# Performance work log

Measured on AMD Instinct MI355X. Metric: run time of the kernel, lower is better.

Reference implementation:

```python
import jax, jax.numpy as jnp
import numpy as np

EPS = 1e-5  # BatchNorm eps (eval mode: running_mean=0, running_var=1)
N, VIEWS, T, V, C_IN, H, W = 8, 4, 5, 17, 18, 16, 16
C_HID = 16


def _bn(y, g, b):
    # eval-mode BatchNorm2d on channel axis 3 of (b, g, v, c, h, w)
    s = (g / jnp.sqrt(1.0 + EPS)).reshape(1, 1, 1, -1, 1, 1)
    return y * s + b.reshape(1, 1, 1, -1, 1, 1)


def _st_gcn_layer(x, A_sp, A_tm, A_vw, Wg_k, bg_k, g1, b1, Wt_k, bt_k, g2, b2, residual):
    """One st_gcn block over 7 relation types. x: (N, Views, T, V, C, H, W)."""
    n, vw, t, v, c, h, w = x.shape
    outs = []
    for k in range(7):  # fixed small set of relations
        if k < 4:  # root/close/further/sym: graph axis is V
            xk = x.reshape(n, vw * t, v, c, h, w)
            A = A_sp[k]
        elif k < 6:  # forward/backward: graph axis is T
            xk = jnp.swapaxes(x, 2, 3).reshape(n, vw * v, t, c, h, w)
            A = A_tm[k - 4]
        else:  # n_views: graph axis is Views
            xk = jnp.swapaxes(x.reshape(n, vw, t * v, c, h, w), 1, 2)
            A = A_vw
        res = xk if residual else 0.0
        # HeatmapGraphical: 1x1 conv then adjacency aggregation over graph axis
        y = jnp.einsum('oc,bgvchw->bgvohw', Wg_k[k], xk) + bg_k[k].reshape(1, 1, 1, -1, 1, 1)
        y = jnp.einsum('uv,bgvohw->bguohw', A, y)
        # tcn: BN -> ReLU -> 1x1 conv -> BN, + residual
        y = jax.nn.relu(_bn(y, g1[k], b1[k]))
        y = jnp.einsum('oc,bgvchw->bgvohw', Wt_k[k], y) + bt_k[k].reshape(1, 1, 1, -1, 1, 1)
        y = _bn(y, g2[k], b2[k]) + res
        o = y.shape[3]
        if k < 4:
            yk = y.reshape(n, vw, t, v, o, h, w)
        elif k < 6:
            yk = jnp.swapaxes(y.reshape(n, vw, v, t, o, h, w), 2, 3)
        else:
            yk = jnp.swapaxes(y, 1, 2).reshape(n, vw, t, v, o, h, w)
        outs.append(yk)
    return jax.nn.relu(sum(outs))


def setup_inputs() -> dict:
    key = jax.random.key(0)
    ks = jax.random.split(key, 14)
    return {
        'x': jax.random.normal(ks[0], (N, VIEWS, T, V, C_IN, H, W), jnp.float32),
        'A_sp': jax.random.uniform(ks[1], (4, V, V), jnp.float32),
        'A_tm': jax.random.uniform(ks[2], (2, T, T), jnp.float32),
        'A_vw': jax.random.uniform(ks[3], (VIEWS, VIEWS), jnp.float32),
        'Wg0': jax.random.normal(ks[4], (7, C_HID, C_IN), jnp.float32) * 0.1,
        'bg0': jax.random.normal(ks[5], (7, C_HID), jnp.float32) * 0.1,
        'Wg': jax.random.normal(ks[6], (2, 7, C_HID, C_HID), jnp.float32) * 0.1,
        'bg': jax.random.normal(ks[7], (2, 7, C_HID), jnp.float32) * 0.1,
        'bn1g': jax.random.uniform(ks[8], (3, 7, C_HID), jnp.float32, 0.5, 1.5),
        'bn1b': jax.random.normal(ks[9], (3, 7, C_HID), jnp.float32) * 0.1,
        'Wt': jax.random.normal(ks[10], (3, 7, C_HID, C_HID), jnp.float32) * 0.1,
        'bt': jax.random.normal(ks[11], (3, 7, C_HID), jnp.float32) * 0.1,
        'bn2g': jax.random.uniform(ks[12], (3, 7, C_HID), jnp.float32, 0.5, 1.5),
        'bn2b': jax.random.normal(ks[13], (3, 7, C_HID), jnp.float32) * 0.1,
    }


def reference(x, A_sp, A_tm, A_vw, Wg0, bg0, Wg, bg, bn1g, bn1b, Wt, bt, bn2g, bn2b):
    # Layer 0: 18->16, residual=False (ZerosMapping)
    y = _st_gcn_layer(x, A_sp, A_tm, A_vw, Wg0, bg0, bn1g[0], bn1b[0], Wt[0], bt[0], bn2g[0], bn2b[0], residual=False)
    # Layers 1, 2: 16->16, residual=Identity
    for l in range(2):
        y = _st_gcn_layer(y, A_sp, A_tm, A_vw, Wg[l], bg[l], bn1g[l + 1], bn1b[l + 1], Wt[l + 1], bt[l + 1], bn2g[l + 1], bn2b[l + 1], residual=True)
    return y
```

## Files before the change

### kernel.cpp

```cpp
#include <hip/hip_runtime.h>
#include <hip/hip_bf16.h>

typedef __attribute__((ext_vector_type(8))) short bf16x8;
typedef __attribute__((ext_vector_type(4))) float f32x4;
typedef unsigned short ush;

constexpr int NODESV = 340, CIN = 18;
constexpr int GRP = 20;
constexpr int NSLOT = 400;
constexpr int NTILE = 25;
constexpr int RS1 = 412;
constexpr int SLX = 3208;
constexpr int SL8 = 3200;
constexpr int PC = 6120;
constexpr int PCP = 6144;
constexpr int QN = 5440;

constexpr int    WS_SB_F  = 21 * 16;
constexpr int    WS_WG    = 1536;
constexpr int    WS_WT    = WS_WG + 21 * 64 * 8 * 2;
constexpr int    WS_ASP   = WS_WT + 21 * 64 * 8 * 2;
constexpr int    WS_R16   = WS_ASP + 4096;
constexpr size_t WS_XT    = 65536;
constexpr size_t WS_NEED  = WS_XT + (size_t)8 * 256 * PCP * 2;

__device__ __forceinline__ ush f2bf(float f) {
    union { __hip_bfloat16 h; ush u; } c; c.h = __float2bfloat16(f); return c.u;
}
__device__ __forceinline__ float bf2f(ush s) {
    return __uint_as_float((unsigned)s << 16);
}
__device__ __forceinline__ unsigned pkbf2(float lo, float hi) {
    union { __hip_bfloat162 h; unsigned u; } c;
    c.h = __float22bfloat162_rn(make_float2(lo, hi));
    return c.u;
}

__global__ void stgcn_prep(
    const float* __restrict__ Asp,
    const float* __restrict__ Wg0, const float* __restrict__ bg0,
    const float* __restrict__ Wgx, const float* __restrict__ bgx,
    const float* __restrict__ g1,  const float* __restrict__ b1,
    const float* __restrict__ Wt,  const float* __restrict__ bt,
    const float* __restrict__ g2,  const float* __restrict__ b2,
    void* __restrict__ ws)
{
    const int lk = blockIdx.x;
    const int l = lk / 7, k = lk % 7;
    const int lane = threadIdx.x;
    const int o = lane & 15, quad = lane >> 4;
    float* bgvA = (float*)ws;
    float* SbA  = bgvA + WS_SB_F;
    ush* wgF = (ush*)((char*)ws + WS_WG);
    ush* wtF = (ush*)((char*)ws + WS_WT);
    const float rs = 1.0f / sqrtf(1.0f + 1e-5f);
    const float s1 = g1[lk * 16 + o] * rs;
    const float s2 = g2[lk * 16 + o] * rs;

    unsigned wg4[4], wt4[4];
    #pragma unroll
    for (int i2 = 0; i2 < 4; ++i2) {
        int c0 = quad * 8 + i2 * 2, c1 = c0 + 1;
        float a0, a1;
        if (l == 0) {
            a0 = (c0 < 18) ? Wg0[(k * 16 + o) * 18 + c0] * s1 : 0.f;
            a1 = (c1 < 18) ? Wg0[(k * 16 + o) * 18 + c1] * s1 : 0.f;
        } else {
            a0 = (c0 < 16) ? Wgx[(((l - 1) * 7 + k) * 16 + o) * 16 + c0] * s1 : 0.f;
            a1 = (c1 < 16) ? Wgx[(((l - 1) * 7 + k) * 16 + o) * 16 + c1] * s1 : 0.f;
        }
        float t0 = (c0 < 16) ? Wt[(lk * 16 + o) * 16 + c0] * s2 : 0.f;
        float t1 = (c1 < 16) ? Wt[(lk * 16 + o) * 16 + c1] * s2 : 0.f;
        wg4[i2] = pkbf2(a0, a1);
        wt4[i2] = pkbf2(t0, t1);
    }
    *(uint4*)&wgF[(lk * 64 + lane) * 8] = make_uint4(wg4[0], wg4[1], wg4[2], wg4[3]);
    *(uint4*)&wtF[(lk * 64 + lane) * 8] = make_uint4(wt4[0], wt4[1], wt4[2], wt4[3]);
    if (quad == 0)
        bgvA[lk * 16 + o] = ((l == 0) ? bg0[k * 16 + o] : bgx[((l - 1) * 7 + k) * 16 + o]) * s1;
    if (lk == 0 && lane < 48) {
        int ll = lane >> 4, ch = lane & 15;
        float s = 0.f;
        for (int kk = 0; kk < 7; ++kk) {
            int q = (ll * 7 + kk) * 16 + ch;
            s += bt[q] * (g2[q] * rs) + b2[q];
        }
        SbA[ll * 16 + ch] = s;
    }
    if (lk < 4) {
        ush* aspF = (ush*)((char*)ws + WS_ASP);
        ush* r16F = (ush*)((char*)ws + WS_R16);
        bf16x8 a0 = {};
        #pragma unroll
        for (int i = 0; i < 8; ++i) {
            int v = quad * 8 + i;
            a0[i] = (short)((v < 17) ? f2bf(Asp[(lk * 17 + o) * 17 + v]) : 0);
        }
        *(bf16x8*)&aspF[(lk * 64 + lane) * 8] = a0;
        if (lane < 32)
            r16F[lk * 32 + lane] = (lane < 17) ? f2bf(Asp[(lk * 17 + 16) * 17 + lane]) : (ush)0;
    }
}

__global__ __launch_bounds__(256) void stgcn_tin(const float* __restrict__ x,
                                                 void* __restrict__ ws)
{
    __shared__ float tf[32][256];
    const int b = blockIdx.x, tid = threadIdx.x;
    const int n = b & 7, pc0 = (b >> 3) * 32;
    for (int j = 0; j < 32; ++j) {
        int pc = pc0 + j;
        tf[j][tid] = (pc < PC) ? x[((size_t)n * PC + pc) * 256 + tid] : 0.f;
    }
    __syncthreads();
    ush* dst = (ush*)((char*)ws + WS_XT) + (size_t)(n * 256 + tid) * PCP + pc0;
    unsigned pk[16];
    #pragma unroll
    for (int j2 = 0; j2 < 16; ++j2) pk[j2] = pkbf2(tf[2 * j2][tid], tf[2 * j2 + 1][tid]);
    #pragma unroll
    for (int q4 = 0; q4 < 4; ++q4)
        *(uint4*)&dst[q4 * 8] = make_uint4(pk[q4*4], pk[q4*4+1], pk[q4*4+2], pk[q4*4+3]);
}

__global__ __launch_bounds__(256) void stgcn_tout_bf(const void* __restrict__ ws,
                                                     float* __restrict__ out)
{
    __shared__ ush tg[32][256];
    const int b = blockIdx.x, tid = threadIdx.x;
    const int n = b & 7, q0 = (b >> 3) * 32;
    const ush* src = (const ush*)((const char*)ws + WS_XT) + (size_t)(n * 256 + tid) * PCP + q0;
    #pragma unroll
    for (int j4 = 0; j4 < 4; ++j4) {
        uint4 v = *(const uint4*)&src[j4 * 8];
        unsigned u[4] = {v.x, v.y, v.z, v.w};
        #pragma unroll
        for (int e = 0; e < 4; ++e) {
            tg[j4*8 + e*2 + 0][tid] = (ush)(u[e] & 0xffffu);
            tg[j4*8 + e*2 + 1][tid] = (ush)(u[e] >> 16);
        }
    }
    __syncthreads();
    for (int j = 0; j < 32; ++j)
        out[((size_t)n * QN + q0 + j) * 256 + tid] = bf2f(tg[j][tid]);
}

template<int TP>
__global__ __launch_bounds__(512, 2) void stgcn_main(
    const float* __restrict__ x,
    const float* __restrict__ Asp_g, const float* __restrict__ Atm_g, const float* __restrict__ Avw_g,
    const float* __restrict__ b1, void* __restrict__ ws,
    float* __restrict__ out)
{
    __shared__ __align__(16) ush xsb[2 * SLX];
    __shared__ __align__(16) ush xs2[NSLOT * 2];
    __shared__ __align__(16) ush z1g[16 * RS1];
    __shared__ __align__(16) ush z2s[2 * SL8];

    const int tid  = threadIdx.x;
    const int wv   = tid >> 6;
    const int lane = tid & 63;
    const int o    = tid & 15;
    const int quad = (tid >> 4) & 3;
    const int w16  = tid >> 4;
    const int bid  = blockIdx.x;
    const int n = bid & 7, hw = bid >> 3;

    const float* bgvA = (const float*)ws;
    const float* SbA  = bgvA + WS_SB_F;
    const ush* wgF  = (const ush*)((const char*)ws + WS_WG);
    const ush* wtF  = (const ush*)((const char*)ws + WS_WT);
    const ush* aspF = (const ush*)((const char*)ws + WS_ASP);
    const ush* r16F = (const ush*)((const char*)ws + WS_R16);

    for (int i = tid; i < SLX; i += 512) ((unsigned*)xsb)[i] = 0u;
    for (int i = tid; i < NSLOT; i += 512) ((unsigned*)xs2)[i] = 0u;
    for (int i = tid; i < (16 * RS1) / 2; i += 512) ((unsigned*)z1g)[i] = 0u;
    for (int i = tid; i < SL8; i += 512) ((unsigned*)z2s)[i] = 0u;
    __syncthreads();

    if (TP) {
        const ush* xrow = (const ush*)((const char*)ws + WS_XT) + (size_t)(n * 256 + hw) * PCP;
        for (int i = tid; i < PC; i += 512) {
            int p = i / CIN, c = i - p * CIN;
            int slot = p + 3 * (p / 17);
            if (c < 16) xsb[(c >> 3) * SLX + slot * 8 + (c & 7)] = xrow[i];
            else        xs2[slot * 2 + (c - 16)] = xrow[i];
        }
    } else {
        const float* xb = x + (size_t)n * PC * 256 + hw;
        for (int i = tid; i < PC; i += 512) {
            int p = i / CIN, c = i - p * CIN;
            int slot = p + 3 * (p / 17);
            ush v = f2bf(xb[(size_t)i * 256]);
            if (c < 16) xsb[(c >> 3) * SLX + slot * 8 + (c & 7)] = v;
            else        xs2[slot * 2 + (c - 16)] = v;
        }
    }
    __syncthreads();

    f32x4 acc[4];

    #pragma unroll 1
    for (int l = 0; l < 3; ++l) {
        #pragma unroll
        for (int t = 0; t < 4; ++t) {
            int tile = t * 8 + wv;
            f32x4 z = {0.f, 0.f, 0.f, 0.f};
            acc[t] = z;
            if (l > 0 && tile < NTILE) {
                int node = tile * 16 + o;
                uint2 w = *(const uint2*)&xsb[(quad >> 1) * SLX + node * 8 + (quad & 1) * 4];
                acc[t][0] = 7.f * bf2f((ush)(w.x & 0xffffu));
                acc[t][1] = 7.f * bf2f((ush)(w.x >> 16));
                acc[t][2] = 7.f * bf2f((ush)(w.y & 0xffffu));
                acc[t][3] = 7.f * bf2f((ush)(w.y >> 16));
            }
        }

        #pragma unroll 1
        for (int k = 0; k < 7; ++k) {
            const int lk = l * 7 + k;
            bf16x8 wg = *(const bf16x8*)&wgF[(lk * 64 + lane) * 8];
            bf16x8 wt = *(const bf16x8*)&wtF[(lk * 64 + lane) * 8];
            const float bgv = bgvA[lk * 16 + o];

            #pragma unroll
            for (int t = 0; t < 4; ++t) {
                int tile = t * 8 + wv;
                if (tile < NTILE) {
                    int node = tile * 16 + o;
                    bf16x8 xa = {};
                    if (quad < 2) {
                        xa = *(const bf16x8*)&xsb[quad * SLX + node * 8];
                    } else if (quad == 2 && l == 0) {
                        unsigned w2 = *(const unsigned*)&xs2[node * 2];
                        xa[0] = (short)(ush)(w2 & 0xffffu);
                        xa[1] = (short)(ush)(w2 >> 16);
                    }
                    f32x4 z = {bgv, bgv, bgv, bgv};
                    z = __builtin_amdgcn_mfma_f32_16x16x32_bf16(xa, wg, z, 0, 0, 0);
                    *(uint2*)&z1g[o * RS1 + tile * 16 + quad * 4] =
                        make_uint2(pkbf2(z[0], z[1]), pkbf2(z[2], z[3]));
                }
            }
            __syncthreads();

            if (k < 4) {
                bf16x8 aA = *(const bf16x8*)&aspF[(k * 64 + lane) * 8];
                bf16x8 aB = {};
                if (o == 0) aB = *(const bf16x8*)&r16F[k * 32 + quad * 8];
                float4 b1q = *(const float4*)&b1[lk * 16 + quad * 4];
                #pragma unroll
                for (int gi = 0; gi < 3; ++gi) {
                    int grp = gi * 8 + wv;
                    if (grp < 20) {
                        bf16x8 bz = *(const bf16x8*)&z1g[o * RS1 + grp * GRP + quad * 8];
                        f32x4 y0 = {b1q.x, b1q.y, b1q.z, b1q.w};
                        y0 = __builtin_amdgcn_mfma_f32_16x16x32_bf16(bz, aA, y0, 0, 0, 0);
                        f32x4 y1 = {b1q.x, b1q.y, b1q.z, b1q.w};
                        y1 = __builtin_amdgcn_mfma_f32_16x16x32_bf16(bz, aB, y1, 0, 0, 0);
                        *(uint2*)&z2s[(quad >> 1) * SL8 + (grp * GRP + o) * 8 + (quad & 1) * 4] =
                            make_uint2(pkbf2(fmaxf(y0[0], 0.f), fmaxf(y0[1], 0.f)),
                                       pkbf2(fmaxf(y0[2], 0.f), fmaxf(y0[3], 0.f)));
                        if (o == 0) {
                            *(uint2*)&z2s[(quad >> 1) * SL8 + (grp * GRP + 16) * 8 + (quad & 1) * 4] =
                                make_uint2(pkbf2(fmaxf(y1[0], 0.f), fmaxf(y1[1], 0.f)),
                                           pkbf2(fmaxf(y1[2], 0.f), fmaxf(y1[3], 0.f)));
                        }
                    }
                }
            } else if (k < 6) {
                const float b1v = b1[lk * 16 + o];
                const float* Ar = Atm_g + (k - 4) * 25;
                #pragma unroll
                for (int j = 0; j < 3; ++j) {
                    int g = w16 + 32 * j;
                    if (g < 68) {
                        int vw = g / 17, v = g - vw * 17;
                        float vals[5];
                        #pragma unroll
                        for (int t2 = 0; t2 < 5; ++t2)
                            vals[t2] = bf2f(z1g[o * RS1 + vw * 100 + t2 * GRP + v]);
                        #pragma unroll
                        for (int tp = 0; tp < 5; ++tp) {
                            float y = b1v;
                            #pragma unroll
                            for (int t2 = 0; t2 < 5; ++t2)
                                y = fmaf(Ar[tp * 5 + t2], vals[t2], y);
                            z2s[(o >> 3) * SL8 + ((vw * 5 + tp) * GRP + v) * 8 + (o & 7)] =
                                f2bf(fmaxf(y, 0.f));
                        }
                    }
                }
            } else {
                const float b1v = b1[lk * 16 + o];
                #pragma unroll
                for (int j = 0; j < 3; ++j) {
                    int g = w16 + 32 * j;
                    if (g < 85) {
                        int tt = g / 17, v = g - tt * 17;
                        float vals[4];
                        #pragma unroll
                        for (int vw = 0; vw < 4; ++vw)
                            vals[vw] = bf2f(z1g[o * RS1 + vw * 100 + tt * GRP + v]);
                        #pragma unroll
                        for (int vp = 0; vp < 4; ++vp) {
                            float y = b1v;
                            #pragma unroll
                            for (int vw = 0; vw < 4; ++vw)
                                y = fmaf(Avw_g[vp * 4 + vw], vals[vw], y);
                            z2s[(o >> 3) * SL8 + ((vp * 5 + tt) * GRP + v) * 8 + (o & 7)] =
                                f2bf(fmaxf(y, 0.f));
                        }
                    }
                }
            }
            __syncthreads();

            #pragma unroll
            for (int t = 0; t < 4; ++t) {
                int tile = t * 8 + wv;
                if (tile < NTILE) {
                    int node = tile * 16 + o;
                    bf16x8 za = {};
                    if (quad < 2) za = *(const bf16x8*)&z2s[quad * SL8 + node * 8];
                    acc[t] = __builtin_amdgcn_mfma_f32_16x16x32_bf16(wt, za, acc[t], 0, 0, 0);
                }
            }
        }

        float4 Sb4 = *(const float4*)&SbA[l * 16 + quad * 4];
        if (l < 2) {
            __syncthreads();
            #pragma unroll
            for (int t = 0; t < 4; ++t) {
                int tile = t * 8 + wv;
                if (tile < NTILE) {
                    float v0 = fmaxf(acc[t][0] + Sb4.x, 0.f);
                    float v1 = fmaxf(acc[t][1] + Sb4.y, 0.f);
                    float v2 = fmaxf(acc[t][2] + Sb4.z, 0.f);
                    float v3 = fmaxf(acc[t][3] + Sb4.w, 0.f);
                    int s = tile * 16 + o;
                    *(uint2*)&xsb[(quad >> 1) * SLX + s * 8 + (quad & 1) * 4] =
                        make_uint2(pkbf2(v0, v1), pkbf2(v2, v3));
                }
            }
            __syncthreads();
        } else {
            #pragma unroll
            for (int t = 0; t < 4; ++t) {
                int tile = t * 8 + wv;
                if (tile < NTILE) {
                    int s = tile * 16 + o;
                    int m = s / GRP, vv = s - GRP * m;
                    if (vv < 17) {
                        int p = m * 17 + vv;
                        float r0 = fmaxf(acc[t][0] + Sb4.x, 0.f);
                        float r1 = fmaxf(acc[t][1] + Sb4.y, 0.f);
                        float r2 = fmaxf(acc[t][2] + Sb4.z, 0.f);
                        float r3 = fmaxf(acc[t][3] + Sb4.w, 0.f);
                        if (TP) {
                            ush* osrow = (ush*)((char*)ws + WS_XT) + (size_t)(n * 256 + hw) * PCP;
                            *(uint2*)&osrow[p * 16 + quad * 4] =
                                make_uint2(pkbf2(r0, r1), pkbf2(r2, r3));
                        } else {
                            float* ob = out + ((size_t)((n * NODESV + p) * 16 + quad * 4)) * 256 + hw;
                            ob[0] = r0; ob[256] = r1; ob[512] = r2; ob[768] = r3;
                        }
                    }
                }
            }
        }
    }
}

extern "C" void kernel_launch(void* const* d_in, const int* in_sizes, int n_in,
                              void* d_out, int out_size, void* d_ws, size_t ws_size,
                              hipStream_t stream) {
    const float* x    = (const float*)d_in[0];
    const float* Asp  = (const float*)d_in[1];
    const float* Atm  = (const float*)d_in[2];
    const float* Avw  = (const float*)d_in[3];
    const float* Wg0  = (const float*)d_in[4];
    const float* bg0  = (const float*)d_in[5];
    const float* Wgx  = (const float*)d_in[6];
    const float* bgx  = (const float*)d_in[7];
    const float* g1   = (const float*)d_in[8];
    const float* b1   = (const float*)d_in[9];
    const float* Wt   = (const float*)d_in[10];
    const float* bt   = (const float*)d_in[11];
    const float* g2   = (const float*)d_in[12];
    const float* b2   = (const float*)d_in[13];
    float* out = (float*)d_out;

    stgcn_prep<<<dim3(21), dim3(64), 0, stream>>>(
        Asp, Wg0, bg0, Wgx, bgx, g1, b1, Wt, bt, g2, b2, d_ws);

    if (ws_size >= WS_NEED) {
        stgcn_tin<<<dim3(8 * 192), dim3(256), 0, stream>>>(x, d_ws);
        stgcn_main<1><<<dim3(8 * 256), dim3(512), 0, stream>>>(
            x, Asp, Atm, Avw, b1, d_ws, out);
        stgcn_tout_bf<<<dim3(8 * 170), dim3(256), 0, stream>>>(d_ws, out);
    } else {
        stgcn_main<0><<<dim3(8 * 256), dim3(512), 0, stream>>>(
            x, Asp, Atm, Avw, b1, d_ws, out);
    }
}
```

Baseline: 218.5 us.

## Double-buffer z1/z2 scratch to overlap next relation's graph conv with current

Double-buffers the z1g and z2s shared scratch buffers and software-pipelines the per-relation loop. The first 1x1 conv for relation k+1 is computed right after relation k's adjacency aggregation, so each relation needs one barrier instead of two. This removes a block-wide barrier per relation. In exchange it doubles that LDS footprint, which may hurt occupancy under launch_bounds(512,2), and adds register pressure.

```diff
diff --git a/kernel.cpp b/kernel.cpp
--- a/kernel.cpp
+++ b/kernel.cpp
@@ -12,6 +12,8 @@
 constexpr int RS1 = 412;
 constexpr int SLX = 3208;
 constexpr int SL8 = 3200;
+constexpr int Z1SZ = 16 * RS1;
+constexpr int Z2SZ = 2 * SL8;
 constexpr int PC = 6120;
 constexpr int PCP = 6144;
 constexpr int QN = 5440;
@@ -153,8 +155,8 @@
 {
     __shared__ __align__(16) ush xsb[2 * SLX];
     __shared__ __align__(16) ush xs2[NSLOT * 2];
-    __shared__ __align__(16) ush z1g[16 * RS1];
-    __shared__ __align__(16) ush z2s[2 * SL8];
+    __shared__ __align__(16) ush z1g[2 * Z1SZ];
+    __shared__ __align__(16) ush z2s[2 * Z2SZ];
 
     const int tid  = threadIdx.x;
     const int wv   = tid >> 6;
@@ -174,8 +176,8 @@
 
     for (int i = tid; i < SLX; i += 512) ((unsigned*)xsb)[i] = 0u;
     for (int i = tid; i < NSLOT; i += 512) ((unsigned*)xs2)[i] = 0u;
-    for (int i = tid; i < (16 * RS1) / 2; i += 512) ((unsigned*)z1g)[i] = 0u;
-    for (int i = tid; i < SL8; i += 512) ((unsigned*)z2s)[i] = 0u;
+    for (int i = tid; i < Z1SZ; i += 512) ((unsigned*)z1g)[i] = 0u;
+    for (int i = tid; i < Z2SZ; i += 512) ((unsigned*)z2s)[i] = 0u;
     __syncthreads();
 
     if (TP) {
@@ -217,13 +219,10 @@
             }
         }
 
-        #pragma unroll 1
-        for (int k = 0; k < 7; ++k) {
-            const int lk = l * 7 + k;
-            bf16x8 wg = *(const bf16x8*)&wgF[(lk * 64 + lane) * 8];
-            bf16x8 wt = *(const bf16x8*)&wtF[(lk * 64 + lane) * 8];
-            const float bgv = bgvA[lk * 16 + o];
-
+        {
+            const int lk0 = l * 7;
+            bf16x8 wg = *(const bf16x8*)&wgF[(lk0 * 64 + lane) * 8];
+            const float bgv = bgvA[lk0 * 16 + o];
             #pragma unroll
             for (int t = 0; t < 4; ++t) {
                 int tile = t * 8 + wv;
@@ -243,7 +242,15 @@
                         make_uint2(pkbf2(z[0], z[1]), pkbf2(z[2], z[3]));
                 }
             }
-            __syncthreads();
+        }
+        __syncthreads();
+
+        #pragma unroll 1
+        for (int k = 0; k < 7; ++k) {
+            const int lk = l * 7 + k;
+            const int zb = k & 1;
+            const ush* z1c = z1g + zb * Z1SZ;
+            ush* z2c = z2s + zb * Z2SZ;
 
             if (k < 4) {
                 bf16x8 aA = *(const bf16x8*)&aspF[(k * 64 + lane) * 8];
@@ -254,16 +261,16 @@
                 for (int gi = 0; gi < 3; ++gi) {
                     int grp = gi * 8 + wv;
                     if (grp < 20) {
-                        bf16x8 bz = *(const bf16x8*)&z1g[o * RS1 + grp * GRP + quad * 8];
+                        bf16x8 bz = *(const bf16x8*)&z1c[o * RS1 + grp * GRP + quad * 8];
                         f32x4 y0 = {b1q.x, b1q.y, b1q.z, b1q.w};
                         y0 = __builtin_amdgcn_mfma_f32_16x16x32_bf16(bz, aA, y0, 0, 0, 0);
                         f32x4 y1 = {b1q.x, b1q.y, b1q.z, b1q.w};
                         y1 = __builtin_amdgcn_mfma_f32_16x16x32_bf16(bz, aB, y1, 0, 0, 0);
-                        *(uint2*)&z2s[(quad >> 1) * SL8 + (grp * GRP + o) * 8 + (quad & 1) * 4] =
+                        *(uint2*)&z2c[(quad >> 1) * SL8 + (grp * GRP + o) * 8 + (quad & 1) * 4] =
                             make_uint2(pkbf2(fmaxf(y0[0], 0.f), fmaxf(y0[1], 0.f)),
                                        pkbf2(fmaxf(y0[2], 0.f), fmaxf(y0[3], 0.f)));
                         if (o == 0) {
-                            *(uint2*)&z2s[(quad >> 1) * SL8 + (grp * GRP + 16) * 8 + (quad & 1) * 4] =
+                            *(uint2*)&z2c[(quad >> 1) * SL8 + (grp * GRP + 16) * 8 + (quad & 1) * 4] =
                                 make_uint2(pkbf2(fmaxf(y1[0], 0.f), fmaxf(y1[1], 0.f)),
                                            pkbf2(fmaxf(y1[2], 0.f), fmaxf(y1[3], 0.f)));
                         }
@@ -280,14 +287,14 @@
                         float vals[5];
                         #pragma unroll
                         for (int t2 = 0; t2 < 5; ++t2)
-                            vals[t2] = bf2f(z1g[o * RS1 + vw * 100 + t2 * GRP + v]);
+                            vals[t2] = bf2f(z1c[o * RS1 + vw * 100 + t2 * GRP + v]);
                         #pragma unroll
                         for (int tp = 0; tp < 5; ++tp) {
                             float y = b1v;
                             #pragma unroll
                             for (int t2 = 0; t2 < 5; ++t2)
                                 y = fmaf(Ar[tp * 5 + t2], vals[t2], y);
-                            z2s[(o >> 3) * SL8 + ((vw * 5 + tp) * GRP + v) * 8 + (o & 7)] =
+                            z2c[(o >> 3) * SL8 + ((vw * 5 + tp) * GRP + v) * 8 + (o & 7)] =
                                 f2bf(fmaxf(y, 0.f));
                         }
                     }
@@ -302,29 +309,60 @@
                         float vals[4];
                         #pragma unroll
                         for (int vw = 0; vw < 4; ++vw)
-                            vals[vw] = bf2f(z1g[o * RS1 + vw * 100 + tt * GRP + v]);
+                            vals[vw] = bf2f(z1c[o * RS1 + vw * 100 + tt * GRP + v]);
                         #pragma unroll
                         for (int vp = 0; vp < 4; ++vp) {
                             float y = b1v;
                             #pragma unroll
                             for (int vw = 0; vw < 4; ++vw)
                                 y = fmaf(Avw_g[vp * 4 + vw], vals[vw], y);
-                            z2s[(o >> 3) * SL8 + ((vp * 5 + tt) * GRP + v) * 8 + (o & 7)] =
+                            z2c[(o >> 3) * SL8 + ((vp * 5 + tt) * GRP + v) * 8 + (o & 7)] =
                                 f2bf(fmaxf(y, 0.f));
                         }
                     }
                 }
             }
+
+            __builtin_amdgcn_sched_barrier(0);
+
+            if (k < 6) {
+                const int lk1 = lk + 1;
+                ush* z1n = z1g + (zb ^ 1) * Z1SZ;
+                bf16x8 wg = *(const bf16x8*)&wgF[(lk1 * 64 + lane) * 8];
+                const float bgv = bgvA[lk1 * 16 + o];
+                #pragma unroll
+                for (int t = 0; t < 4; ++t) {
+                    int tile = t * 8 + wv;
+                    if (tile < NTILE) {
+                        int node = tile * 16 + o;
+                        bf16x8 xa = {};
+                        if (quad < 2) {
+                            xa = *(const bf16x8*)&xsb[quad * SLX + node * 8];
+                        } else if (quad == 2 && l == 0) {
+                            unsigned w2 = *(const unsigned*)&xs2[node * 2];
+                            xa[0] = (short)(ush)(w2 & 0xffffu);
+                            xa[1] = (short)(ush)(w2 >> 16);
+                        }
+                        f32x4 z = {bgv, bgv, bgv, bgv};
+                        z = __builtin_amdgcn_mfma_f32_16x16x32_bf16(xa, wg, z, 0, 0, 0);
+                        *(uint2*)&z1n[o * RS1 + tile * 16 + quad * 4] =
+                            make_uint2(pkbf2(z[0], z[1]), pkbf2(z[2], z[3]));
+                    }
+                }
+            }
             __syncthreads();
 
-            #pragma unroll
-            for (int t = 0; t < 4; ++t) {
-                int tile = t * 8 + wv;
-                if (tile < NTILE) {
-                    int node = tile * 16 + o;
-                    bf16x8 za = {};
-                    if (quad < 2) za = *(const bf16x8*)&z2s[quad * SL8 + node * 8];
-                    acc[t] = __builtin_amdgcn_mfma_f32_16x16x32_bf16(wt, za, acc[t], 0, 0, 0);
+            {
+                bf16x8 wt = *(const bf16x8*)&wtF[(lk * 64 + lane) * 8];
+                #pragma unroll
+                for (int t = 0; t < 4; ++t) {
+                    int tile = t * 8 + wv;
+                    if (tile < NTILE) {
+                        int node = tile * 16 + o;
+                        bf16x8 za = {};
+                        if (quad < 2) za = *(const bf16x8*)&z2c[quad * SL8 + node * 8];
+                        acc[t] = __builtin_amdgcn_mfma_f32_16x16x32_bf16(wt, za, acc[t], 0, 0, 0);
+                    }
                 }
             }
         }
```

After: 244.2 us. 1.12x slower.
